# Optimization experiments

Hardware: AMD Instinct MI355X
Metric: run time of the kernel (lower is better)

## Reference

```python
import jax, jax.numpy as jnp
import numpy as np

LN_EPS = 1e-5

def setup_inputs() -> dict:
    key = jax.random.key(0)
    k1, k2, k3 = jax.random.split(key, 3)
    L, B, D = 2048, 8, 1024
    x = jax.random.normal(k1, (L, B, D), dtype=jnp.float32)
    c = jnp.zeros((B, D), dtype=jnp.float32)
    W = jax.random.normal(k2, (D, 3 * D), dtype=jnp.float32) * 0.02
    # bias init from _init_bias: u-bias 0, f-bias 0.5, r-bias 0
    b = jnp.concatenate([jnp.zeros(D), jnp.full((D,), 0.5), jnp.zeros(D)]).astype(jnp.float32)
    gamma = jnp.ones((D,), dtype=jnp.float32)
    beta = jnp.zeros((D,), dtype=jnp.float32)
    return {"x": x, "c": c, "W": W, "b": b, "gamma": gamma, "beta": beta}

def reference(x, c, W, b, gamma, beta):
    # LayerNorm over last dim
    mu = jnp.mean(x, axis=-1, keepdims=True)
    var = jnp.mean(jnp.square(x - mu), axis=-1, keepdims=True)
    x_norm = (x - mu) * jax.lax.rsqrt(var + LN_EPS) * gamma + beta
    # Fused u/f/r projection: [L,B,3D]
    ufr = jnp.einsum('lbd,de->lbe', x_norm, W) + b
    u, f, r = jnp.split(ufr, 3, axis=-1)
    f_gate = jax.nn.sigmoid(f)
    r_gate = jax.nn.sigmoid(r)
    # Linear recurrence c_t = f_t * c_{t-1} + (1-f_t) * u_t via scan over time
    def step(c_prev, fu):
        f_t, u_t = fu
        c_t = f_t * c_prev + (1.0 - f_t) * u_t
        return c_t, c_t
    last_c, c_stack = jax.lax.scan(step, c, (f_gate, u))
    hs = r_gate * jnp.tanh(c_stack) + (1.0 - r_gate) * x_norm
    return x + hs, last_c
```

## Files before the change

kernel.cpp:

```cpp
#include <hip/hip_runtime.h>
#include <hip/hip_bf16.h>


typedef unsigned short u16;
typedef __bf16 bf16x8 __attribute__((ext_vector_type(8)));
typedef float f32x4 __attribute__((ext_vector_type(4)));

#define L_DIM 2048
#define B_DIM 8
#define D_DIM 1024
#define M_DIM (L_DIM * B_DIM)
#define K_DIM D_DIM
#define N_DIM (3 * D_DIM)
#define NCH 32
#define CLEN (L_DIM / NCH)
#define NT (K_DIM / 64)

#define LDS_B_OFF 65536
#define LDS_TOTAL 81920

__device__ __forceinline__ float bf2f(u16 h) {
    unsigned int u = ((unsigned int)h) << 16;
    float f;
    __builtin_memcpy(&f, &u, 4);
    return f;
}

__device__ __forceinline__ u16 f2bf(float f) {
    unsigned int u;
    __builtin_memcpy(&u, &f, 4);
    u = u + 0x7fff + ((u >> 16) & 1);
    return (u16)(u >> 16);
}

__device__ __forceinline__ void async16(void* lds, const void* g) {
    __builtin_amdgcn_global_load_lds(
        (const __attribute__((address_space(1))) void*)g,
        (__attribute__((address_space(3))) void*)lds, 16, 0, 0);
}

__global__ __launch_bounds__(256) void ln_kernel(const float* __restrict__ x,
                                                 const float* __restrict__ gamma,
                                                 const float* __restrict__ beta,
                                                 u16* __restrict__ xn,
                                                 float2* __restrict__ mrs) {
    int row = blockIdx.x;
    int tid = threadIdx.x;
    const float4* xr = (const float4*)(x + (size_t)row * D_DIM);
    float4 v = xr[tid];
    float s = v.x + v.y + v.z + v.w;
    float q = v.x * v.x + v.y * v.y + v.z * v.z + v.w * v.w;
    #pragma unroll
    for (int off = 32; off; off >>= 1) {
        s += __shfl_down(s, off);
        q += __shfl_down(q, off);
    }
    __shared__ float ss[4], qq[4];
    int lane = tid & 63, wv = tid >> 6;
    if (lane == 0) { ss[wv] = s; qq[wv] = q; }
    __syncthreads();
    s = ss[0] + ss[1] + ss[2] + ss[3];
    q = qq[0] + qq[1] + qq[2] + qq[3];
    float mu = s * (1.0f / D_DIM);
    float var = q * (1.0f / D_DIM) - mu * mu;
    float rs = rsqrtf(var + 1e-5f);
    if (tid == 0) mrs[row] = make_float2(mu, rs);
    float4 g = ((const float4*)gamma)[tid];
    float4 bt = ((const float4*)beta)[tid];
    ushort4 o;
    o.x = f2bf((v.x - mu) * rs * g.x + bt.x);
    o.y = f2bf((v.y - mu) * rs * g.y + bt.y);
    o.z = f2bf((v.z - mu) * rs * g.z + bt.z);
    o.w = f2bf((v.w - mu) * rs * g.w + bt.w);
    ((ushort4*)(xn + (size_t)row * D_DIM))[tid] = o;
}

__global__ __launch_bounds__(256) void wt_kernel(const float* __restrict__ W,
                                                 u16* __restrict__ Wt) {
    __shared__ float t[64][65];
    int k0 = blockIdx.x * 64;
    int n0 = blockIdx.y * 64;
    int col = threadIdx.x & 63;
    int rg4 = threadIdx.x >> 6;
    #pragma unroll
    for (int j = 0; j < 16; ++j) {
        int r = rg4 * 16 + j;
        t[r][col] = W[(size_t)(k0 + r) * N_DIM + n0 + col];
    }
    __syncthreads();
    #pragma unroll
    for (int j = 0; j < 16; ++j) {
        int nr = rg4 * 16 + j;
        Wt[(size_t)(n0 + nr) * K_DIM + k0 + col] = f2bf(t[col][nr]);
    }
}

__global__ __launch_bounds__(512, 4) void gemm_kernel(const u16* __restrict__ A,
                                                      const u16* __restrict__ Bt,
                                                      const float* __restrict__ bias,
                                                      u16* __restrict__ uo,
                                                      u16* __restrict__ fo,
                                                      u16* __restrict__ ro) {
    extern __shared__ char lds[];
    const int tid = threadIdx.x;
    const int wave = tid >> 6, lane = tid & 63;
    const int lm = lane & 15, lg = lane >> 4;
    const int wm = wave >> 2, wn = wave & 3;
    const int m0 = blockIdx.x * 256;
    const int n0 = blockIdx.y * 128;

    const int xk0 = ((0 | lg) ^ (lm & 7)) << 4;
    const int xk1 = ((4 | lg) ^ (lm & 7)) << 4;
    const char* pA0 = lds + (wm * 128 + lm) * 128 + xk0;
    const char* pA1 = lds + (wm * 128 + lm) * 128 + xk1;
    const char* pB0 = lds + LDS_B_OFF + (wn * 32 + lm) * 128 + xk0;
    const char* pB1 = lds + LDS_B_OFF + (wn * 32 + lm) * 128 + xk1;

    const int c1 = 512 + tid;
    const int r0 = tid >> 3, cc0 = (tid & 7) ^ (r0 & 7);
    const int r1 = c1 >> 3, cc1 = (c1 & 7) ^ (r1 & 7);
    const char* gA0 = (const char*)A + ((size_t)(m0 + r0) * K_DIM + cc0 * 8) * 2;
    const char* gA1 = (const char*)A + ((size_t)(m0 + r1) * K_DIM + cc1 * 8) * 2;
    const char* gB0 = (const char*)Bt + ((size_t)(n0 + r0) * K_DIM + cc0 * 8) * 2;
    const char* gB1 = (const char*)Bt + ((size_t)(n0 + r1) * K_DIM + cc1 * 8) * 2;
    char* dstW = lds + wave * 1024;

    f32x4 acc[8][2] = {};
    bf16x8 av[4], aw[4], bv0[2], bv1[2];

    auto stageA = [&](int t1, int h) {
        if (t1 >= NT) return;
        char* dst = dstW + ((t1 & 1) << 15) + (h << 14);
        int ko = ((t1 & 15) << 7) + (h << 18);
        async16(dst,        gA0 + ko);
        async16(dst + 8192, gA1 + ko);
    };
    auto stageB = [&](int t1) {
        if (t1 >= NT) return;
        char* dst = dstW + LDS_B_OFF;
        int ko = (t1 & 15) << 7;
        async16(dst,        gB0 + ko);
        async16(dst + 8192, gB1 + ko);
    };

#define LDA(dst, pbase, bb, mf0)                                                \
    do { _Pragma("unroll")                                                      \
        for (int q = 0; q < 4; ++q)                                             \
            dst[q] = *(const bf16x8*)(pbase + (bb) * 32768 + ((mf0) + q) * 2048); \
    } while (0)

#define LDB(dst, pbase)                                                         \
    do { _Pragma("unroll")                                                      \
        for (int nf = 0; nf < 2; ++nf)                                          \
            dst[nf] = *(const bf16x8*)(pbase + nf * 2048);                      \
    } while (0)

#define MFMA8(r0q, afr, bfr)                                                    \
    do { _Pragma("unroll")                                                      \
        for (int q = 0; q < 4; ++q)                                             \
            _Pragma("unroll")                                                   \
            for (int nf = 0; nf < 2; ++nf)                                      \
                acc[(r0q) + q][nf] = __builtin_amdgcn_mfma_f32_16x16x32_bf16(   \
                    afr[q], bfr[nf], acc[(r0q) + q][nf], 0, 0, 0);              \
    } while (0)

#define PH_SYNC()                                                               \
    do { __builtin_amdgcn_s_barrier();                                          \
         asm volatile("s_waitcnt lgkmcnt(0)");                                  \
         __builtin_amdgcn_sched_barrier(0); } while (0)

#define TILE_BODY(t, bb)                                                        \
    do {                                                                        \
                                                                   \
        LDA(av, pA0, bb, 0);                                                    \
        LDB(bv0, pB0);                                                          \
        stageA((t) + 1, 0);                                                     \
        PH_SYNC();                                                              \
        __builtin_amdgcn_s_setprio(1);  MFMA8(0, av, bv0);                      \
        __builtin_amdgcn_s_setprio(0);  __builtin_amdgcn_s_barrier();           \
                                                                   \
        LDA(av, pA1, bb, 0);                                                    \
        LDB(bv1, pB1);                                                          \
        stageA((t) + 1, 1);                                                     \
        PH_SYNC();                                                              \
        __builtin_amdgcn_s_setprio(1);  MFMA8(0, av, bv1);                      \
        __builtin_amdgcn_s_setprio(0);  __builtin_amdgcn_s_barrier();           \
                          \
        LDA(aw, pA0, bb, 4);                                                    \
        stageB((t) + 1);                                                        \
        PH_SYNC();                                                              \
        __builtin_amdgcn_s_setprio(1);  MFMA8(4, aw, bv0);                      \
        __builtin_amdgcn_s_setprio(0);  __builtin_amdgcn_s_barrier();           \
                                                                   \
        LDA(aw, pA1, bb, 4);                                                    \
        PH_SYNC();                                                              \
        __builtin_amdgcn_s_setprio(1);  MFMA8(4, aw, bv1);                      \
        __builtin_amdgcn_s_setprio(0);                                          \
        asm volatile("s_waitcnt vmcnt(0)" ::: "memory");                        \
        __builtin_amdgcn_s_barrier();                                           \
    } while (0)

    stageA(0, 0); stageA(0, 1); stageB(0);
    asm volatile("s_waitcnt vmcnt(0)" ::: "memory");
    __builtin_amdgcn_s_barrier();

    #pragma unroll 1
    for (int t = 0; t < NT; t += 2) {
        TILE_BODY(t, 0);
        TILE_BODY(t + 1, 1);
    }

    int seg = n0 >> 10;
    u16* outp = (seg == 0) ? uo : ((seg == 1) ? fo : ro);
    float bb2[2];
    #pragma unroll
    for (int nf = 0; nf < 2; ++nf) bb2[nf] = bias[n0 + wn * 32 + nf * 16 + lm];
    const int cmb = (n0 + wn * 32 + lm) & 1023;
    #pragma unroll
    for (int mf = 0; mf < 8; ++mf) {
        #pragma unroll
        for (int j = 0; j < 4; ++j) {
            int row = m0 + wm * 128 + mf * 16 + lg * 4 + j;
            u16* rp = outp + (size_t)row * D_DIM + cmb;
            #pragma unroll
            for (int nf = 0; nf < 2; ++nf) {
                float val = acc[mf][nf][j] + bb2[nf];
                if (seg != 0) val = 1.0f / (1.0f + __expf(-val));
                rp[nf * 16] = f2bf(val);
            }
        }
    }
#undef LDA
#undef LDB
#undef MFMA8
#undef PH_SYNC
#undef TILE_BODY
}

__global__ __launch_bounds__(256) void scan1_kernel(const u16* __restrict__ fg,
                                                    const u16* __restrict__ u,
                                                    float* __restrict__ Aa,
                                                    float* __restrict__ Ss) {
    int ch = blockIdx.x;
    int bd = (blockIdx.y * 256 + threadIdx.x) * 2;
    int b = bd >> 10, d = bd & 1023;
    float a0 = 1.0f, a1 = 1.0f, s0 = 0.0f, s1 = 0.0f;
    for (int t = ch * CLEN; t < ch * CLEN + CLEN; ++t) {
        size_t idx = ((size_t)(t * B_DIM + b) << 10) + d;
        ushort2 f2 = *(const ushort2*)(fg + idx);
        ushort2 u2 = *(const ushort2*)(u + idx);
        float f0 = bf2f(f2.x), f1 = bf2f(f2.y);
        float v0 = bf2f(u2.x), v1 = bf2f(u2.y);
        s0 = f0 * s0 + (1.0f - f0) * v0;
        s1 = f1 * s1 + (1.0f - f1) * v1;
        a0 *= f0;
        a1 *= f1;
    }
    int o = ch * 8192 + bd;
    *(float2*)(Aa + o) = make_float2(a0, a1);
    *(float2*)(Ss + o) = make_float2(s0, s1);
}

__global__ __launch_bounds__(256) void scan2_kernel(const float* __restrict__ Aa,
                                                    const float* __restrict__ Ss,
                                                    const float* __restrict__ c0,
                                                    float* __restrict__ cs,
                                                    float* __restrict__ lastc) {
    int bd = blockIdx.x * 256 + threadIdx.x;
    float c = c0[bd];
    #pragma unroll 4
    for (int ch = 0; ch < NCH; ++ch) {
        cs[ch * 8192 + bd] = c;
        c = Aa[ch * 8192 + bd] * c + Ss[ch * 8192 + bd];
    }
    lastc[bd] = c;
}

__global__ __launch_bounds__(256) void scan3_kernel(const float* __restrict__ cs,
                                                    const u16* __restrict__ fg,
                                                    const u16* __restrict__ u,
                                                    const u16* __restrict__ rg,
                                                    const float2* __restrict__ mrs,
                                                    const float* __restrict__ gamma,
                                                    const float* __restrict__ beta,
                                                    const float* __restrict__ x,
                                                    float* __restrict__ out) {
    int ch = blockIdx.x;
    int bd = (blockIdx.y * 256 + threadIdx.x) * 2;
    int b = bd >> 10, d = bd & 1023;
    float2 gm = *(const float2*)(gamma + d);
    float2 bt = *(const float2*)(beta + d);
    float c0v = cs[ch * 8192 + bd];
    float c1v = cs[ch * 8192 + bd + 1];
    for (int t = ch * CLEN; t < ch * CLEN + CLEN; ++t) {
        size_t idx = ((size_t)(t * B_DIM + b) << 10) + d;
        ushort2 f2 = *(const ushort2*)(fg + idx);
        ushort2 u2 = *(const ushort2*)(u + idx);
        ushort2 r2 = *(const ushort2*)(rg + idx);
        float2 x2 = *(const float2*)(x + idx);
        float2 mr = mrs[t * B_DIM + b];
        float f0 = bf2f(f2.x), f1 = bf2f(f2.y);
        float v0 = bf2f(u2.x), v1 = bf2f(u2.y);
        float r0 = bf2f(r2.x), r1 = bf2f(r2.y);
        float n0 = (x2.x - mr.x) * mr.y * gm.x + bt.x;
        float n1 = (x2.y - mr.x) * mr.y * gm.y + bt.y;
        c0v = f0 * c0v + (1.0f - f0) * v0;
        c1v = f1 * c1v + (1.0f - f1) * v1;
        float h0 = r0 * tanhf(c0v) + (1.0f - r0) * n0;
        float h1 = r1 * tanhf(c1v) + (1.0f - r1) * n1;
        *(float2*)(out + idx) = make_float2(x2.x + h0, x2.y + h1);
    }
}

extern "C" void kernel_launch(void* const* d_in, const int* in_sizes, int n_in,
                              void* d_out, int out_size, void* d_ws, size_t ws_size,
                              hipStream_t stream) {
    const float* x     = (const float*)d_in[0];
    const float* c0    = (const float*)d_in[1];
    const float* W     = (const float*)d_in[2];
    const float* b     = (const float*)d_in[3];
    const float* gamma = (const float*)d_in[4];
    const float* beta  = (const float*)d_in[5];
    float* out = (float*)d_out;
    float* lastc = out + (size_t)M_DIM * D_DIM;

    char* w = (char*)d_ws;
    u16* xn = (u16*)w;  w += (size_t)M_DIM * D_DIM * 2;
    u16* Wt = (u16*)w;  w += (size_t)N_DIM * K_DIM * 2;
    u16* ug = (u16*)w;  w += (size_t)M_DIM * D_DIM * 2;
    u16* fg = (u16*)w;  w += (size_t)M_DIM * D_DIM * 2;
    u16* rg = (u16*)w;  w += (size_t)M_DIM * D_DIM * 2;
    float* Aa = (float*)w; w += (size_t)NCH * 8192 * 4;
    float* Ss = (float*)w; w += (size_t)NCH * 8192 * 4;
    float* cs = (float*)w; w += (size_t)NCH * 8192 * 4;
    float2* mrs = (float2*)w; w += (size_t)M_DIM * 8;

    hipFuncSetAttribute(reinterpret_cast<const void*>(gemm_kernel),
                        hipFuncAttributeMaxDynamicSharedMemorySize, LDS_TOTAL);

    ln_kernel<<<M_DIM, 256, 0, stream>>>(x, gamma, beta, xn, mrs);
    wt_kernel<<<dim3(K_DIM / 64, N_DIM / 64), 256, 0, stream>>>(W, Wt);
    gemm_kernel<<<dim3(M_DIM / 256, N_DIM / 128), 512, LDS_TOTAL, stream>>>(xn, Wt, b, ug, fg, rg);
    scan1_kernel<<<dim3(NCH, 16), 256, 0, stream>>>(fg, ug, Aa, Ss);
    scan2_kernel<<<32, 256, 0, stream>>>(Aa, Ss, c0, cs, lastc);
    scan3_kernel<<<dim3(NCH, 16), 256, 0, stream>>>(cs, fg, ug, rg, mrs, gamma, beta, x, out);
}
```

Before: 206.9 us.

## Reshape GEMM wave tiling from 128x32 to 64x64 per wave

Changes the GEMM's 8-wave arrangement from 2x4 to 4x2, so each wave computes a square 64x64 output tile instead of a tall 128x32 one. Per K-tile this cuts LDS fragment loads per wave (8 A plus 8 B instead of 16 A plus 4 B). It also drops one of the four phase syncs and reorganizes the B fragment registers to four per k-half. The cost is that more B fragment registers stay live, which may affect register pressure at the 4-block launch bound.

```diff
diff --git a/kernel.cpp b/kernel.cpp
--- a/kernel.cpp
+++ b/kernel.cpp
@@ -105,16 +105,16 @@
     const int tid = threadIdx.x;
     const int wave = tid >> 6, lane = tid & 63;
     const int lm = lane & 15, lg = lane >> 4;
-    const int wm = wave >> 2, wn = wave & 3;
+    const int wm = wave >> 1, wn = wave & 1;
     const int m0 = blockIdx.x * 256;
     const int n0 = blockIdx.y * 128;
 
     const int xk0 = ((0 | lg) ^ (lm & 7)) << 4;
     const int xk1 = ((4 | lg) ^ (lm & 7)) << 4;
-    const char* pA0 = lds + (wm * 128 + lm) * 128 + xk0;
-    const char* pA1 = lds + (wm * 128 + lm) * 128 + xk1;
-    const char* pB0 = lds + LDS_B_OFF + (wn * 32 + lm) * 128 + xk0;
-    const char* pB1 = lds + LDS_B_OFF + (wn * 32 + lm) * 128 + xk1;
+    const char* pA0 = lds + (wm * 64 + lm) * 128 + xk0;
+    const char* pA1 = lds + (wm * 64 + lm) * 128 + xk1;
+    const char* pB0 = lds + LDS_B_OFF + (wn * 64 + lm) * 128 + xk0;
+    const char* pB1 = lds + LDS_B_OFF + (wn * 64 + lm) * 128 + xk1;
 
     const int c1 = 512 + tid;
     const int r0 = tid >> 3, cc0 = (tid & 7) ^ (r0 & 7);
@@ -125,8 +125,8 @@
     const char* gB1 = (const char*)Bt + ((size_t)(n0 + r1) * K_DIM + cc1 * 8) * 2;
     char* dstW = lds + wave * 1024;
 
-    f32x4 acc[8][2] = {};
-    bf16x8 av[4], aw[4], bv0[2], bv1[2];
+    f32x4 acc[4][4] = {};
+    bf16x8 av[4], aw[4], bv0[4], bv1[4];
 
     auto stageA = [&](int t1, int h) {
         if (t1 >= NT) return;
@@ -143,25 +143,19 @@
         async16(dst + 8192, gB1 + ko);
     };
 
-#define LDA(dst, pbase, bb, mf0)                                                \
+#define LD4(dst, pbase, boff)                                                   \
     do { _Pragma("unroll")                                                      \
         for (int q = 0; q < 4; ++q)                                             \
-            dst[q] = *(const bf16x8*)(pbase + (bb) * 32768 + ((mf0) + q) * 2048); \
+            dst[q] = *(const bf16x8*)((pbase) + (boff) + q * 2048);             \
     } while (0)
 
-#define LDB(dst, pbase)                                                         \
-    do { _Pragma("unroll")                                                      \
-        for (int nf = 0; nf < 2; ++nf)                                          \
-            dst[nf] = *(const bf16x8*)(pbase + nf * 2048);                      \
-    } while (0)
-
-#define MFMA8(r0q, afr, bfr)                                                    \
+#define MFMA2(afr, bfr, nfb)                                                    \
     do { _Pragma("unroll")                                                      \
         for (int q = 0; q < 4; ++q)                                             \
             _Pragma("unroll")                                                   \
             for (int nf = 0; nf < 2; ++nf)                                      \
-                acc[(r0q) + q][nf] = __builtin_amdgcn_mfma_f32_16x16x32_bf16(   \
-                    afr[q], bfr[nf], acc[(r0q) + q][nf], 0, 0, 0);              \
+                acc[q][(nfb) + nf] = __builtin_amdgcn_mfma_f32_16x16x32_bf16(   \
+                    afr[q], bfr[(nfb) + nf], acc[q][(nfb) + nf], 0, 0, 0);      \
     } while (0)
 
 #define PH_SYNC()                                                               \
@@ -172,29 +166,26 @@
 #define TILE_BODY(t, bb)                                                        \
     do {                                                                        \
                                                                    \
-        LDA(av, pA0, bb, 0);                                                    \
-        LDB(bv0, pB0);                                                          \
+        LD4(av, pA0, (bb) * 32768);                                             \
+        LD4(bv0, pB0, 0);                                                       \
         stageA((t) + 1, 0);                                                     \
         PH_SYNC();                                                              \
-        __builtin_amdgcn_s_setprio(1);  MFMA8(0, av, bv0);                      \
+        __builtin_amdgcn_s_setprio(1);  MFMA2(av, bv0, 0);                      \
         __builtin_amdgcn_s_setprio(0);  __builtin_amdgcn_s_barrier();           \
                                                                    \
-        LDA(av, pA1, bb, 0);                                                    \
-        LDB(bv1, pB1);                                                          \
+        LD4(bv1, pB1, 0);                                                       \
         stageA((t) + 1, 1);                                                     \
         PH_SYNC();                                                              \
-        __builtin_amdgcn_s_setprio(1);  MFMA8(0, av, bv1);                      \
+        __builtin_amdgcn_s_setprio(1);  MFMA2(av, bv0, 2);                      \
         __builtin_amdgcn_s_setprio(0);  __builtin_amdgcn_s_barrier();           \
-                          \
-        LDA(aw, pA0, bb, 4);                                                    \
+             \
+        LD4(aw, pA1, (bb) * 32768);                                             \
         stageB((t) + 1);                                                        \
         PH_SYNC();                                                              \
-        __builtin_amdgcn_s_setprio(1);  MFMA8(4, aw, bv0);                      \
+        __builtin_amdgcn_s_setprio(1);  MFMA2(aw, bv1, 0);                      \
         __builtin_amdgcn_s_setprio(0);  __builtin_amdgcn_s_barrier();           \
-                                                                   \
-        LDA(aw, pA1, bb, 4);                                                    \
-        PH_SYNC();                                                              \
-        __builtin_amdgcn_s_setprio(1);  MFMA8(4, aw, bv1);                      \
+                                                         \
+        __builtin_amdgcn_s_setprio(1);  MFMA2(aw, bv1, 2);                      \
         __builtin_amdgcn_s_setprio(0);                                          \
         asm volatile("s_waitcnt vmcnt(0)" ::: "memory");                        \
         __builtin_amdgcn_s_barrier();                                           \
@@ -212,27 +203,26 @@
 
     int seg = n0 >> 10;
     u16* outp = (seg == 0) ? uo : ((seg == 1) ? fo : ro);
-    float bb2[2];
-    #pragma unroll
-    for (int nf = 0; nf < 2; ++nf) bb2[nf] = bias[n0 + wn * 32 + nf * 16 + lm];
-    const int cmb = (n0 + wn * 32 + lm) & 1023;
-    #pragma unroll
-    for (int mf = 0; mf < 8; ++mf) {
+    float bb4[4];
+    #pragma unroll
+    for (int nf = 0; nf < 4; ++nf) bb4[nf] = bias[n0 + wn * 64 + nf * 16 + lm];
+    const int cmb = (n0 + wn * 64 + lm) & 1023;
+    #pragma unroll
+    for (int mf = 0; mf < 4; ++mf) {
         #pragma unroll
         for (int j = 0; j < 4; ++j) {
-            int row = m0 + wm * 128 + mf * 16 + lg * 4 + j;
+            int row = m0 + wm * 64 + mf * 16 + lg * 4 + j;
             u16* rp = outp + (size_t)row * D_DIM + cmb;
             #pragma unroll
-            for (int nf = 0; nf < 2; ++nf) {
-                float val = acc[mf][nf][j] + bb2[nf];
+            for (int nf = 0; nf < 4; ++nf) {
+                float val = acc[mf][nf][j] + bb4[nf];
                 if (seg != 0) val = 1.0f / (1.0f + __expf(-val));
                 rp[nf * 16] = f2bf(val);
             }
         }
     }
-#undef LDA
-#undef LDB
-#undef MFMA8
+#undef LD4
+#undef MFMA2
 #undef PH_SYNC
 #undef TILE_BODY
 }
```

After: 267.9 us. 1.29x slower.
